# Kernel optimization log

Hardware: AMD Instinct MI355X
Metric: run time of the kernel (lower is better)

## Reference

```python
import jax, jax.numpy as jnp
import numpy as np

B, T, DQ, DV, A, F, K = 64, 1024, 1024, 512, 512, 32, 31


def setup_inputs() -> dict:
    key = jax.random.key(0)
    ks = jax.random.split(key, 8)
    query = jax.random.normal(ks[0], (B, DQ), jnp.float32)
    values = jax.random.normal(ks[1], (B, T, DV), jnp.float32)
    # decoder-step states (as produced by init_states)
    attention_cum = jnp.zeros((B, T), jnp.float32)
    attention_old = jnp.zeros((B, T), jnp.float32)
    alpha = jnp.concatenate([jnp.ones((B, 1), jnp.float32),
                             jnp.zeros((B, T - 1), jnp.float32) + 1e-7], axis=1)
    # learned parameters (Glorot-ish scaling)
    W_query = jax.random.normal(ks[2], (DQ, A), jnp.float32) / np.sqrt(DQ)
    W_inputs = jax.random.normal(ks[3], (DV, A), jnp.float32) / np.sqrt(DV)
    v_w = jax.random.normal(ks[4], (A, 1), jnp.float32) / np.sqrt(A)
    v_b = jnp.zeros((1,), jnp.float32)
    loc_kernel = jax.random.normal(ks[5], (K, 2, F), jnp.float32) / np.sqrt(K * 2)  # WIO
    W_loc = jax.random.normal(ks[6], (F, A), jnp.float32) / np.sqrt(F)
    return {"query": query, "values": values, "attention_cum": attention_cum,
            "attention_old": attention_old, "alpha": alpha,
            "W_query": W_query, "W_inputs": W_inputs, "v_w": v_w, "v_b": v_b,
            "loc_kernel": loc_kernel, "W_loc": W_loc}


def reference(query, values, attention_cum, attention_old, alpha,
              W_query, W_inputs, v_w, v_b, loc_kernel, W_loc):
    # process_values: cached projection of encoder memory  [B,T,A]
    processed_values = jnp.einsum('btd,da->bta', values, W_inputs)
    # location features: conv over stacked (old, cum) attention  [B,T,2]->[B,T,F]
    attn_cat = jnp.stack([attention_old, attention_cum], axis=2)
    conv = jax.lax.conv_general_dilated(attn_cat, loc_kernel, window_strides=(1,),
                                        padding='SAME',
                                        dimension_numbers=('NWC', 'WIO', 'NWC'))
    processed_attn = jnp.einsum('btf,fa->bta', conv, W_loc)
    # query projection  [B,1,A]
    processed_query = (query @ W_query)[:, None, :]
    # additive score  [B,T]
    score = (jnp.tanh(processed_values + processed_query + processed_attn) @ v_w)[..., 0] + v_b
    scores_norm = jax.nn.softmax(score, axis=-1)
    # forward attention recursion
    fwd_shifted = jnp.pad(alpha[:, :-1], ((0, 0), (1, 0)))
    new_alpha = (0.5 * alpha + 0.5 * fwd_shifted + 1e-8) * scores_norm
    new_alpha = new_alpha / jnp.sum(new_alpha, axis=1, keepdims=True)
    attn_weights = new_alpha
    # updated states
    new_cum = attention_cum + scores_norm
    new_old = attn_weights
    # context vector  [B,DV]
    context = jnp.einsum('bt,btd->bd', attn_weights, values)
    return (context, attn_weights, new_cum, new_old, new_alpha)
```

## Files before the change

### kernel.cpp

```cpp
#include <hip/hip_runtime.h>
#include <hip/hip_bf16.h>
#include <cstdint>
#include <cstddef>

#define B 64
#define T 1024
#define DQ 1024
#define DV 512
#define A_DIM 512
#define F_DIM 32
#define KW 31
#define M_TOT (B*T)
#define KEXT 544
#define NCHUNK 17

typedef __attribute__((ext_vector_type(8))) short short8;
typedef __attribute__((ext_vector_type(4))) float f32x4;
typedef __attribute__((ext_vector_type(16))) float f32x16;

static __device__ __forceinline__ unsigned short f2bf(float f) {
    unsigned int u = __builtin_bit_cast(unsigned int, f);
    u += 0x7fffu + ((u >> 16) & 1u);
    return (unsigned short)(u >> 16);
}

static __device__ __forceinline__ float tanh_fast(float x) {
    float e = __expf(2.0f * x);
    return 1.0f - 2.0f * __builtin_amdgcn_rcpf(e + 1.0f);
}

__global__ void pq_kernel(const float* __restrict__ query, const float* __restrict__ Wq,
                          float* __restrict__ pq, float* __restrict__ score) {
    __shared__ float red[4][64];
    int gid = blockIdx.x * 256 + threadIdx.x;
    if (gid < M_TOT) score[gid] = 0.f;
    int b = blockIdx.x >> 3, a0 = (blockIdx.x & 7) * 64;
    int al = threadIdx.x & 63, ks = threadIdx.x >> 6;
    const float* qr = query + (size_t)b * DQ + ks * 256;
    const float* wc = Wq + (size_t)(ks * 256) * A_DIM + a0 + al;
    float acc = 0.f;
    #pragma unroll 8
    for (int k = 0; k < 256; ++k) acc += qr[k] * wc[(size_t)k * A_DIM];
    red[ks][al] = acc;
    __syncthreads();
    if (ks == 0) {
        float s = red[0][al] + red[1][al] + red[2][al] + red[3][al];
        pq[b * A_DIM + a0 + al] = s;
    }
}

__global__ void bt_kernel(const float* __restrict__ Wi, const float* __restrict__ Wl,
                          unsigned short* __restrict__ Bt) {
    int a = blockIdx.x;
    for (int k = threadIdx.x; k < KEXT; k += 256) {
        float v = (k < DV) ? Wi[(size_t)k * A_DIM + a] : Wl[(size_t)(k - DV) * A_DIM + a];
        Bt[(size_t)a * KEXT + k] = f2bf(v);
    }
}

__global__ void conv_kernel(const float* __restrict__ old_, const float* __restrict__ cum_,
                            const float* __restrict__ lk, unsigned short* __restrict__ convb) {
    __shared__ float sOld[158], sCum[158];
    __shared__ float sLK[KW * 2 * F_DIM];
    int b = blockIdx.x >> 3, t0 = (blockIdx.x & 7) * 128;
    int tid = threadIdx.x;
    for (int j = tid; j < 158; j += 128) {
        int tt = t0 - 15 + j;
        bool ok = (tt >= 0 && tt < T);
        sOld[j] = ok ? old_[b * T + tt] : 0.f;
        sCum[j] = ok ? cum_[b * T + tt] : 0.f;
    }
    for (int j = tid; j < KW * 2 * F_DIM; j += 128) sLK[j] = lk[j];
    __syncthreads();
    float acc[F_DIM];
    #pragma unroll
    for (int f = 0; f < F_DIM; ++f) acc[f] = 0.f;
    for (int k = 0; k < KW; ++k) {
        float o = sOld[tid + k], c = sCum[tid + k];
        const float* lo = &sLK[(k * 2 + 0) * F_DIM];
        const float* lc = &sLK[(k * 2 + 1) * F_DIM];
        #pragma unroll
        for (int f = 0; f < F_DIM; ++f) acc[f] += o * lo[f] + c * lc[f];
    }
    unsigned short* dst = convb + (size_t)(b * T + t0 + tid) * F_DIM;
    #pragma unroll
    for (int f = 0; f < F_DIM; ++f) dst[f] = f2bf(acc[f]);
}

__launch_bounds__(256, 2)
__global__ void gemm_score(const float* __restrict__ values,
                           const unsigned short* __restrict__ Bt,
                           const unsigned short* __restrict__ convb,
                           const float* __restrict__ pq,
                           const float* __restrict__ vw,
                           float* __restrict__ score) {
    __shared__ __align__(16) short sA[128 * 40];
    __shared__ __align__(16) short sB[256 * 40];
    __shared__ float sPQ[256];
    __shared__ float sVW[256];
    int tid = threadIdx.x;
    int mt = blockIdx.x >> 1, ch = blockIdx.x & 1;
    int m0 = mt * 128, n0 = ch * 256;
    int b = m0 >> 10;
    for (int j = tid; j < 256; j += 256) {
        sPQ[j] = pq[b * A_DIM + n0 + j];
        sVW[j] = vw[n0 + j];
    }
    int w = tid >> 6, lane = tid & 63;
    int l31 = lane & 31, lh = lane >> 5;
    int wm = w & 1, wn = w >> 1;
    f32x16 acc[2][4];
    #pragma unroll
    for (int mi = 0; mi < 2; ++mi)
        #pragma unroll
        for (int ni = 0; ni < 4; ++ni) acc[mi][ni] = (f32x16)0.f;

    for (int c = 0; c < NCHUNK; ++c) {
        __syncthreads();
        #pragma unroll
        for (int j = 0; j < 2; ++j) {
            int task = j * 256 + tid;
            int row = task >> 2, seg = task & 3;
            short8 pk;
            if (c < 16) {
                const float* src = values + (size_t)(m0 + row) * DV + c * 32 + seg * 8;
                float4 x0 = *(const float4*)src;
                float4 x1 = *(const float4*)(src + 4);
                pk[0] = (short)f2bf(x0.x); pk[1] = (short)f2bf(x0.y);
                pk[2] = (short)f2bf(x0.z); pk[3] = (short)f2bf(x0.w);
                pk[4] = (short)f2bf(x1.x); pk[5] = (short)f2bf(x1.y);
                pk[6] = (short)f2bf(x1.z); pk[7] = (short)f2bf(x1.w);
            } else {
                pk = *(const short8*)(const void*)(convb + (size_t)(m0 + row) * F_DIM + seg * 8);
            }
            *(short8*)&sA[row * 40 + seg * 8] = pk;
        }
        #pragma unroll
        for (int j = 0; j < 4; ++j) {
            int task = j * 256 + tid;
            int ar = task >> 2, seg = task & 3;
            short8 pk = *(const short8*)(const void*)(Bt + (size_t)(n0 + ar) * KEXT + c * 32 + seg * 8);
            *(short8*)&sB[ar * 40 + seg * 8] = pk;
        }
        __syncthreads();
        #pragma unroll
        for (int kk = 0; kk < 2; ++kk) {
            short8 af[2], bf[4];
            #pragma unroll
            for (int mi = 0; mi < 2; ++mi)
                af[mi] = *(const short8*)&sA[(wm * 64 + mi * 32 + l31) * 40 + kk * 16 + lh * 8];
            #pragma unroll
            for (int ni = 0; ni < 4; ++ni)
                bf[ni] = *(const short8*)&sB[(wn * 128 + ni * 32 + l31) * 40 + kk * 16 + lh * 8];
            #pragma unroll
            for (int mi = 0; mi < 2; ++mi)
                #pragma unroll
                for (int ni = 0; ni < 4; ++ni)
                    acc[mi][ni] = __builtin_amdgcn_mfma_f32_32x32x16_bf16(af[mi], bf[ni], acc[mi][ni], 0, 0, 0);
        }
    }
    #pragma unroll
    for (int mi = 0; mi < 2; ++mi) {
        #pragma unroll
        for (int r = 0; r < 16; ++r) {
            float s = 0.f;
            #pragma unroll
            for (int ni = 0; ni < 4; ++ni) {
                int bcol = wn * 128 + ni * 32 + l31;
                float x = acc[mi][ni][r] + sPQ[bcol];
                s += tanh_fast(x) * sVW[bcol];
            }
            #pragma unroll
            for (int off = 1; off < 32; off <<= 1) s += __shfl_xor(s, off, 64);
            if (l31 == 0) {
                int row = wm * 64 + mi * 32 + (r & 3) + 8 * (r >> 2) + 4 * lh;
                atomicAdd(&score[m0 + row], s);
            }
        }
    }
}

__global__ void softmax_fwd(const float* __restrict__ score,
                            const float* __restrict__ alpha,
                            const float* __restrict__ cum,
                            float* __restrict__ out) {
    int b = blockIdx.x, t = threadIdx.x;
    __shared__ float sred[16];
    __shared__ float sbc;
    float sc = score[b * T + t];
    int wid = t >> 6, lane = t & 63;
    float m = sc;
    #pragma unroll
    for (int off = 32; off; off >>= 1) m = fmaxf(m, __shfl_xor(m, off, 64));
    if (lane == 0) sred[wid] = m;
    __syncthreads();
    if (t == 0) { float mm = sred[0]; for (int i = 1; i < 16; ++i) mm = fmaxf(mm, sred[i]); sbc = mm; }
    __syncthreads();
    float M = sbc;
    float e = __expf(sc - M);
    float s = e;
    #pragma unroll
    for (int off = 32; off; off >>= 1) s += __shfl_xor(s, off, 64);
    __syncthreads();
    if (lane == 0) sred[wid] = s;
    __syncthreads();
    if (t == 0) { float ss = 0.f; for (int i = 0; i < 16; ++i) ss += sred[i]; sbc = ss; }
    __syncthreads();
    float sn = e / sbc;
    float a_t = alpha[b * T + t];
    float a_p = (t > 0) ? alpha[b * T + t - 1] : 0.f;
    float ua = (0.5f * (a_t + a_p) + 1e-8f) * sn;
    float u = ua;
    #pragma unroll
    for (int off = 32; off; off >>= 1) u += __shfl_xor(u, off, 64);
    __syncthreads();
    if (lane == 0) sred[wid] = u;
    __syncthreads();
    if (t == 0) { float ss = 0.f; for (int i = 0; i < 16; ++i) ss += sred[i]; sbc = ss; }
    __syncthreads();
    float wgt = ua / sbc;
    float* attnw  = out + B * DV;
    float* ncum   = attnw + B * T;
    float* nold   = ncum + B * T;
    float* nalpha = nold + B * T;
    attnw[b * T + t]  = wgt;
    ncum[b * T + t]   = cum[b * T + t] + sn;
    nold[b * T + t]   = wgt;
    nalpha[b * T + t] = wgt;
    if (t < DV) out[b * DV + t] = 0.f;
}

__global__ void context_kernel(const float* __restrict__ values, float* __restrict__ out) {
    const float* attnw = out + B * DV;
    int bid = blockIdx.x;
    int b = bid >> 5, r = bid & 31, dh = r & 1, sl = r >> 1;
    int d = dh * 256 + threadIdx.x;
    float acc = 0.f;
    int tbase = sl * 64;
    #pragma unroll 4
    for (int tt = 0; tt < 64; ++tt) {
        int t = tbase + tt;
        acc += attnw[b * T + t] * values[(size_t)(b * T + t) * DV + d];
    }
    atomicAdd(&out[b * DV + d], acc);
}

extern "C" void kernel_launch(void* const* d_in, const int* in_sizes, int n_in,
                              void* d_out, int out_size, void* d_ws, size_t ws_size,
                              hipStream_t stream) {
    const float* query  = (const float*)d_in[0];
    const float* values = (const float*)d_in[1];
    const float* cum    = (const float*)d_in[2];
    const float* old_   = (const float*)d_in[3];
    const float* alpha  = (const float*)d_in[4];
    const float* Wq     = (const float*)d_in[5];
    const float* Wi     = (const float*)d_in[6];
    const float* vw     = (const float*)d_in[7];
    const float* lk     = (const float*)d_in[9];
    const float* Wl     = (const float*)d_in[10];
    float* out = (float*)d_out;
    char* ws = (char*)d_ws;
    float* ws_pq            = (float*)(ws);
    float* ws_score         = (float*)(ws + 131072);
    unsigned short* ws_Bt   = (unsigned short*)(ws + 393216);
    unsigned short* ws_conv = (unsigned short*)(ws + 1048576);

    pq_kernel<<<512, 256, 0, stream>>>(query, Wq, ws_pq, ws_score);
    bt_kernel<<<512, 256, 0, stream>>>(Wi, Wl, ws_Bt);
    conv_kernel<<<512, 128, 0, stream>>>(old_, cum, lk, ws_conv);
    gemm_score<<<1024, 256, 0, stream>>>(values, ws_Bt, ws_conv, ws_pq, vw, ws_score);
    softmax_fwd<<<64, 1024, 0, stream>>>(ws_score, alpha, cum, out);
    context_kernel<<<2048, 256, 0, stream>>>(values, out);
}
```

Measured before the change: 307.9 us.

## Pre-convert values to bf16, retile score GEMM with LDS DMA, vectorize context

Adds a pass that converts values to bf16 once in workspace when the workspace is large enough. The score GEMM then streams bf16 tiles through global_load_lds DMA into swizzled, unpadded LDS, using 128x128 tiles with 16x16x32 MFMA and higher occupancy. The weight-transpose kernel now goes through a shared-memory tile, and conv/context kernels are revectorized. The context reduction reads the bf16 copy, which lowers precision relative to fp32 values, and the extra conversion pass adds a full read/write of values.

```diff
diff --git a/kernel.cpp b/kernel.cpp
--- a/kernel.cpp
+++ b/kernel.cpp
@@ -16,7 +16,6 @@
 
 typedef __attribute__((ext_vector_type(8))) short short8;
 typedef __attribute__((ext_vector_type(4))) float f32x4;
-typedef __attribute__((ext_vector_type(16))) float f32x16;
 
 static __device__ __forceinline__ unsigned short f2bf(float f) {
     unsigned int u = __builtin_bit_cast(unsigned int, f);
@@ -24,9 +23,38 @@
     return (unsigned short)(u >> 16);
 }
 
+static __device__ __forceinline__ float bf2f(unsigned short h) {
+    return __builtin_bit_cast(float, (unsigned int)h << 16);
+}
+
+static __device__ __forceinline__ short8 pack8(float4 x0, float4 x1) {
+    short8 pk;
+    pk[0] = (short)f2bf(x0.x); pk[1] = (short)f2bf(x0.y);
+    pk[2] = (short)f2bf(x0.z); pk[3] = (short)f2bf(x0.w);
+    pk[4] = (short)f2bf(x1.x); pk[5] = (short)f2bf(x1.y);
+    pk[6] = (short)f2bf(x1.z); pk[7] = (short)f2bf(x1.w);
+    return pk;
+}
+
 static __device__ __forceinline__ float tanh_fast(float x) {
     float e = __expf(2.0f * x);
     return 1.0f - 2.0f * __builtin_amdgcn_rcpf(e + 1.0f);
+}
+
+#define LDSDMA16(gptr, lptr)                                                        \
+    __builtin_amdgcn_global_load_lds(                                               \
+        (const __attribute__((address_space(1))) void*)(const void*)(gptr),         \
+        (__attribute__((address_space(3))) void*)(void*)(lptr), 16, 0, 0)
+
+__global__ void vconv_kernel(const float* __restrict__ v, unsigned short* __restrict__ vbf) {
+    size_t base = (size_t)blockIdx.x * 8192 + (size_t)threadIdx.x * 8;
+    #pragma unroll
+    for (int j = 0; j < 4; ++j) {
+        size_t idx = base + (size_t)j * 2048;
+        float4 x0 = *(const float4*)(v + idx);
+        float4 x1 = *(const float4*)(v + idx + 4);
+        *(short8*)(vbf + idx) = pack8(x0, x1);
+    }
 }
 
 __global__ void pq_kernel(const float* __restrict__ query, const float* __restrict__ Wq,
@@ -51,131 +79,170 @@
 
 __global__ void bt_kernel(const float* __restrict__ Wi, const float* __restrict__ Wl,
                           unsigned short* __restrict__ Bt) {
-    int a = blockIdx.x;
-    for (int k = threadIdx.x; k < KEXT; k += 256) {
-        float v = (k < DV) ? Wi[(size_t)k * A_DIM + a] : Wl[(size_t)(k - DV) * A_DIM + a];
-        Bt[(size_t)a * KEXT + k] = f2bf(v);
+    __shared__ float tile[64][65];
+    int tid = threadIdx.x;
+    if (blockIdx.x < 64) {
+        int k0 = (blockIdx.x >> 3) * 64, a0 = (blockIdx.x & 7) * 64;
+        int al = tid & 63, ko = tid >> 6;
+        #pragma unroll
+        for (int j = 0; j < 16; ++j) {
+            int kl = j * 4 + ko;
+            tile[kl][al] = Wi[(size_t)(k0 + kl) * A_DIM + a0 + al];
+        }
+        __syncthreads();
+        int kl2 = tid & 63, ao = tid >> 6;
+        #pragma unroll
+        for (int j = 0; j < 16; ++j) {
+            int al2 = j * 4 + ao;
+            Bt[(size_t)(a0 + al2) * KEXT + k0 + kl2] = f2bf(tile[kl2][al2]);
+        }
+    } else {
+        int a0 = (blockIdx.x - 64) * 64;
+        int al = tid & 63, ko = tid >> 6;
+        #pragma unroll
+        for (int j = 0; j < 8; ++j) {
+            int kl = j * 4 + ko;
+            tile[kl][al] = Wl[(size_t)kl * A_DIM + a0 + al];
+        }
+        __syncthreads();
+        int kl2 = tid & 31, ao = tid >> 5;
+        #pragma unroll
+        for (int j = 0; j < 8; ++j) {
+            int al2 = j * 8 + ao;
+            Bt[(size_t)(a0 + al2) * KEXT + DV + kl2] = f2bf(tile[kl2][al2]);
+        }
     }
 }
 
 __global__ void conv_kernel(const float* __restrict__ old_, const float* __restrict__ cum_,
                             const float* __restrict__ lk, unsigned short* __restrict__ convb) {
-    __shared__ float sOld[158], sCum[158];
+    __shared__ float sOld[94], sCum[94];
     __shared__ float sLK[KW * 2 * F_DIM];
-    int b = blockIdx.x >> 3, t0 = (blockIdx.x & 7) * 128;
+    int b = blockIdx.x >> 4, t0 = (blockIdx.x & 15) * 64;
     int tid = threadIdx.x;
-    for (int j = tid; j < 158; j += 128) {
+    int tl = tid & 63, fg = tid >> 6;
+    for (int j = tid; j < 94; j += 256) {
         int tt = t0 - 15 + j;
         bool ok = (tt >= 0 && tt < T);
         sOld[j] = ok ? old_[b * T + tt] : 0.f;
         sCum[j] = ok ? cum_[b * T + tt] : 0.f;
     }
-    for (int j = tid; j < KW * 2 * F_DIM; j += 128) sLK[j] = lk[j];
-    __syncthreads();
-    float acc[F_DIM];
-    #pragma unroll
-    for (int f = 0; f < F_DIM; ++f) acc[f] = 0.f;
+    for (int j = tid; j < KW * 2 * F_DIM; j += 256) sLK[j] = lk[j];
+    __syncthreads();
+    float acc[8];
+    #pragma unroll
+    for (int f = 0; f < 8; ++f) acc[f] = 0.f;
     for (int k = 0; k < KW; ++k) {
-        float o = sOld[tid + k], c = sCum[tid + k];
-        const float* lo = &sLK[(k * 2 + 0) * F_DIM];
-        const float* lc = &sLK[(k * 2 + 1) * F_DIM];
-        #pragma unroll
-        for (int f = 0; f < F_DIM; ++f) acc[f] += o * lo[f] + c * lc[f];
-    }
-    unsigned short* dst = convb + (size_t)(b * T + t0 + tid) * F_DIM;
-    #pragma unroll
-    for (int f = 0; f < F_DIM; ++f) dst[f] = f2bf(acc[f]);
-}
-
-__launch_bounds__(256, 2)
+        float o = sOld[tl + k], c = sCum[tl + k];
+        const float* lo = &sLK[(k * 2 + 0) * F_DIM + fg * 8];
+        const float* lc = &sLK[(k * 2 + 1) * F_DIM + fg * 8];
+        #pragma unroll
+        for (int f = 0; f < 8; ++f) acc[f] += o * lo[f] + c * lc[f];
+    }
+    short8 pk;
+    #pragma unroll
+    for (int f = 0; f < 8; ++f) pk[f] = (short)f2bf(acc[f]);
+    *(short8*)(convb + (size_t)(b * T + t0 + tl) * F_DIM + fg * 8) = pk;
+}
+
+template<bool VBF>
+__launch_bounds__(256, 3)
 __global__ void gemm_score(const float* __restrict__ values,
+                           const unsigned short* __restrict__ vbf,
                            const unsigned short* __restrict__ Bt,
                            const unsigned short* __restrict__ convb,
                            const float* __restrict__ pq,
                            const float* __restrict__ vw,
                            float* __restrict__ score) {
-    __shared__ __align__(16) short sA[128 * 40];
-    __shared__ __align__(16) short sB[256 * 40];
-    __shared__ float sPQ[256];
-    __shared__ float sVW[256];
+    __shared__ __align__(16) short sA[128 * 32];
+    __shared__ __align__(16) short sB[128 * 32];
+    __shared__ float sPQ[128];
+    __shared__ float sVW[128];
     int tid = threadIdx.x;
-    int mt = blockIdx.x >> 1, ch = blockIdx.x & 1;
-    int m0 = mt * 128, n0 = ch * 256;
+    int mt = blockIdx.x >> 2, nq = blockIdx.x & 3;
+    int m0 = mt * 128, n0 = nq * 128;
     int b = m0 >> 10;
-    for (int j = tid; j < 256; j += 256) {
-        sPQ[j] = pq[b * A_DIM + n0 + j];
-        sVW[j] = vw[n0 + j];
-    }
-    int w = tid >> 6, lane = tid & 63;
-    int l31 = lane & 31, lh = lane >> 5;
+    if (tid < 128) { sPQ[tid] = pq[b * A_DIM + n0 + tid]; sVW[tid] = vw[n0 + tid]; }
+    int w = tid >> 6, lane = tid & 63, q = lane >> 4, l15 = lane & 15;
     int wm = w & 1, wn = w >> 1;
-    f32x16 acc[2][4];
-    #pragma unroll
-    for (int mi = 0; mi < 2; ++mi)
-        #pragma unroll
-        for (int ni = 0; ni < 4; ++ni) acc[mi][ni] = (f32x16)0.f;
+    f32x4 acc[4][4];
+    #pragma unroll
+    for (int mi = 0; mi < 4; ++mi)
+        #pragma unroll
+        for (int ni = 0; ni < 4; ++ni) acc[mi][ni] = (f32x4)0.f;
+
+    int row0 = tid >> 2,        seg0 = ((tid & 3) - (row0 >> 1)) & 3;
+    int row1 = 64 + (tid >> 2), seg1 = ((tid & 3) - (row1 >> 1)) & 3;
+    int rA = tid >> 1, jA0 = (tid & 1) * 2;
+    int sgA0 = ((jA0 + 0) - (rA >> 1)) & 3;
+    int sgA1 = ((jA0 + 1) - (rA >> 1)) & 3;
 
     for (int c = 0; c < NCHUNK; ++c) {
         __syncthreads();
-        #pragma unroll
-        for (int j = 0; j < 2; ++j) {
-            int task = j * 256 + tid;
-            int row = task >> 2, seg = task & 3;
-            short8 pk;
+        {
+            const unsigned short* g0 = Bt + (size_t)(n0 + row0) * KEXT + c * 32 + seg0 * 8;
+            const unsigned short* g1 = Bt + (size_t)(n0 + row1) * KEXT + c * 32 + seg1 * 8;
+            LDSDMA16(g0, &sB[(0 * 256 + w * 64) * 8]);
+            LDSDMA16(g1, &sB[(1 * 256 + w * 64) * 8]);
+        }
+        if (VBF) {
+            const unsigned short* g0 = (c < 16)
+                ? vbf + (size_t)(m0 + row0) * DV + c * 32 + seg0 * 8
+                : convb + (size_t)(m0 + row0) * F_DIM + seg0 * 8;
+            const unsigned short* g1 = (c < 16)
+                ? vbf + (size_t)(m0 + row1) * DV + c * 32 + seg1 * 8
+                : convb + (size_t)(m0 + row1) * F_DIM + seg1 * 8;
+            LDSDMA16(g0, &sA[(0 * 256 + w * 64) * 8]);
+            LDSDMA16(g1, &sA[(1 * 256 + w * 64) * 8]);
+        } else {
+            short8 p0, p1;
             if (c < 16) {
-                const float* src = values + (size_t)(m0 + row) * DV + c * 32 + seg * 8;
-                float4 x0 = *(const float4*)src;
-                float4 x1 = *(const float4*)(src + 4);
-                pk[0] = (short)f2bf(x0.x); pk[1] = (short)f2bf(x0.y);
-                pk[2] = (short)f2bf(x0.z); pk[3] = (short)f2bf(x0.w);
-                pk[4] = (short)f2bf(x1.x); pk[5] = (short)f2bf(x1.y);
-                pk[6] = (short)f2bf(x1.z); pk[7] = (short)f2bf(x1.w);
+                const float* s0 = values + (size_t)(m0 + rA) * DV + c * 32 + sgA0 * 8;
+                const float* s1 = values + (size_t)(m0 + rA) * DV + c * 32 + sgA1 * 8;
+                p0 = pack8(*(const float4*)s0, *(const float4*)(s0 + 4));
+                p1 = pack8(*(const float4*)s1, *(const float4*)(s1 + 4));
             } else {
-                pk = *(const short8*)(const void*)(convb + (size_t)(m0 + row) * F_DIM + seg * 8);
+                p0 = *(const short8*)(convb + (size_t)(m0 + rA) * F_DIM + sgA0 * 8);
+                p1 = *(const short8*)(convb + (size_t)(m0 + rA) * F_DIM + sgA1 * 8);
             }
-            *(short8*)&sA[row * 40 + seg * 8] = pk;
-        }
-        #pragma unroll
-        for (int j = 0; j < 4; ++j) {
-            int task = j * 256 + tid;
-            int ar = task >> 2, seg = task & 3;
-            short8 pk = *(const short8*)(const void*)(Bt + (size_t)(n0 + ar) * KEXT + c * 32 + seg * 8);
-            *(short8*)&sB[ar * 40 + seg * 8] = pk;
+            *(short8*)&sA[(rA * 4 + jA0 + 0) * 8] = p0;
+            *(short8*)&sA[(rA * 4 + jA0 + 1) * 8] = p1;
         }
         __syncthreads();
-        #pragma unroll
-        for (int kk = 0; kk < 2; ++kk) {
-            short8 af[2], bf[4];
-            #pragma unroll
-            for (int mi = 0; mi < 2; ++mi)
-                af[mi] = *(const short8*)&sA[(wm * 64 + mi * 32 + l31) * 40 + kk * 16 + lh * 8];
+        short8 af[4], bfr[4];
+        #pragma unroll
+        for (int mi = 0; mi < 4; ++mi) {
+            int r = wm * 64 + mi * 16 + l15;
+            int g = (q + (r >> 1)) & 3;
+            af[mi] = *(const short8*)&sA[r * 32 + g * 8];
+        }
+        #pragma unroll
+        for (int ni = 0; ni < 4; ++ni) {
+            int r = wn * 64 + ni * 16 + l15;
+            int g = (q + (r >> 1)) & 3;
+            bfr[ni] = *(const short8*)&sB[r * 32 + g * 8];
+        }
+        #pragma unroll
+        for (int mi = 0; mi < 4; ++mi)
             #pragma unroll
             for (int ni = 0; ni < 4; ++ni)
-                bf[ni] = *(const short8*)&sB[(wn * 128 + ni * 32 + l31) * 40 + kk * 16 + lh * 8];
-            #pragma unroll
-            for (int mi = 0; mi < 2; ++mi)
-                #pragma unroll
-                for (int ni = 0; ni < 4; ++ni)
-                    acc[mi][ni] = __builtin_amdgcn_mfma_f32_32x32x16_bf16(af[mi], bf[ni], acc[mi][ni], 0, 0, 0);
-        }
-    }
-    #pragma unroll
-    for (int mi = 0; mi < 2; ++mi) {
-        #pragma unroll
-        for (int r = 0; r < 16; ++r) {
+                acc[mi][ni] = __builtin_amdgcn_mfma_f32_16x16x32_bf16(af[mi], bfr[ni], acc[mi][ni], 0, 0, 0);
+    }
+    #pragma unroll
+    for (int mi = 0; mi < 4; ++mi) {
+        #pragma unroll
+        for (int r = 0; r < 4; ++r) {
             float s = 0.f;
             #pragma unroll
             for (int ni = 0; ni < 4; ++ni) {
-                int bcol = wn * 128 + ni * 32 + l31;
-                float x = acc[mi][ni][r] + sPQ[bcol];
-                s += tanh_fast(x) * sVW[bcol];
+                int col = wn * 64 + ni * 16 + l15;
+                float x = acc[mi][ni][r] + sPQ[col];
+                s += tanh_fast(x) * sVW[col];
             }
             #pragma unroll
-            for (int off = 1; off < 32; off <<= 1) s += __shfl_xor(s, off, 64);
-            if (l31 == 0) {
-                int row = wm * 64 + mi * 32 + (r & 3) + 8 * (r >> 2) + 4 * lh;
-                atomicAdd(&score[m0 + row], s);
-            }
+            for (int off = 1; off < 16; off <<= 1) s += __shfl_xor(s, off, 64);
+            if (l15 == 0)
+                atomicAdd(&score[m0 + wm * 64 + mi * 16 + q * 4 + r], s);
         }
     }
 }
@@ -230,19 +297,47 @@
     if (t < DV) out[b * DV + t] = 0.f;
 }
 
-__global__ void context_kernel(const float* __restrict__ values, float* __restrict__ out) {
+__global__ void context_kernel(const float* __restrict__ values,
+                               const unsigned short* __restrict__ vbf,
+                               int use_bf, float* __restrict__ out) {
+    __shared__ float red[4][512];
     const float* attnw = out + B * DV;
-    int bid = blockIdx.x;
-    int b = bid >> 5, r = bid & 31, dh = r & 1, sl = r >> 1;
-    int d = dh * 256 + threadIdx.x;
-    float acc = 0.f;
-    int tbase = sl * 64;
-    #pragma unroll 4
-    for (int tt = 0; tt < 64; ++tt) {
-        int t = tbase + tt;
-        acc += attnw[b * T + t] * values[(size_t)(b * T + t) * DV + d];
-    }
-    atomicAdd(&out[b * DV + d], acc);
+    int b = blockIdx.x >> 2, tq = blockIdx.x & 3;
+    int sub = threadIdx.x >> 6, dg = threadIdx.x & 63;
+    int t0 = tq * 256 + sub * 64;
+    float acc[8];
+    #pragma unroll
+    for (int f = 0; f < 8; ++f) acc[f] = 0.f;
+    if (use_bf) {
+        for (int tt = 0; tt < 64; ++tt) {
+            int t = t0 + tt;
+            float wgt = attnw[b * T + t];
+            short8 v = *(const short8*)(vbf + (size_t)(b * T + t) * DV + dg * 8);
+            #pragma unroll
+            for (int f = 0; f < 8; ++f) acc[f] += wgt * bf2f((unsigned short)v[f]);
+        }
+    } else {
+        for (int tt = 0; tt < 64; ++tt) {
+            int t = t0 + tt;
+            float wgt = attnw[b * T + t];
+            const float* src = values + (size_t)(b * T + t) * DV + dg * 8;
+            float4 x0 = *(const float4*)src;
+            float4 x1 = *(const float4*)(src + 4);
+            acc[0] += wgt * x0.x; acc[1] += wgt * x0.y; acc[2] += wgt * x0.z; acc[3] += wgt * x0.w;
+            acc[4] += wgt * x1.x; acc[5] += wgt * x1.y; acc[6] += wgt * x1.z; acc[7] += wgt * x1.w;
+        }
+    }
+    #pragma unroll
+    for (int f = 0; f < 8; ++f) red[sub][dg * 8 + f] = acc[f];
+    __syncthreads();
+    if (sub == 0) {
+        #pragma unroll
+        for (int f = 0; f < 8; ++f) {
+            int d = dg * 8 + f;
+            float s = red[0][d] + red[1][d] + red[2][d] + red[3][d];
+            atomicAdd(&out[b * DV + d], s);
+        }
+    }
 }
 
 extern "C" void kernel_launch(void* const* d_in, const int* in_sizes, int n_in,
@@ -264,11 +359,17 @@
     float* ws_score         = (float*)(ws + 131072);
     unsigned short* ws_Bt   = (unsigned short*)(ws + 393216);
     unsigned short* ws_conv = (unsigned short*)(ws + 1048576);
-
+    unsigned short* ws_vbf  = (unsigned short*)(ws + 8388608);
+    const bool big = ws_size >= (size_t)75497472;
+
+    if (big) vconv_kernel<<<4096, 256, 0, stream>>>(values, ws_vbf);
     pq_kernel<<<512, 256, 0, stream>>>(query, Wq, ws_pq, ws_score);
-    bt_kernel<<<512, 256, 0, stream>>>(Wi, Wl, ws_Bt);
-    conv_kernel<<<512, 128, 0, stream>>>(old_, cum, lk, ws_conv);
-    gemm_score<<<1024, 256, 0, stream>>>(values, ws_Bt, ws_conv, ws_pq, vw, ws_score);
+    bt_kernel<<<72, 256, 0, stream>>>(Wi, Wl, ws_Bt);
+    conv_kernel<<<1024, 256, 0, stream>>>(old_, cum, lk, ws_conv);
+    if (big)
+        gemm_score<true><<<2048, 256, 0, stream>>>(values, ws_vbf, ws_Bt, ws_conv, ws_pq, vw, ws_score);
+    else
+        gemm_score<false><<<2048, 256, 0, stream>>>(values, ws_vbf, ws_Bt, ws_conv, ws_pq, vw, ws_score);
     softmax_fwd<<<64, 1024, 0, stream>>>(ws_score, alpha, cum, out);
-    context_kernel<<<2048, 256, 0, stream>>>(values, out);
-}
+    context_kernel<<<256, 256, 0, stream>>>(values, ws_vbf, big ? 1 : 0, out);
+}
```

Measured after the change: 328.7 us. 1.07x slower.
